# Performance work log

Hardware: AMD Instinct MI355X
Metric: run time of the kernel (lower is better)

Reference implementation:

```python
import jax, jax.numpy as jnp
import numpy as np

WS = 8   # window_size
SS = 4   # shift_size
NH = 4   # num_heads


def _window_partition(x, w):
    B, H, W, C = x.shape
    x = x.reshape(B, H // w, w, W // w, w, C).transpose(0, 1, 3, 2, 4, 5)
    return x.reshape(-1, w, w, C)


def _window_reverse(win, w, H, W):
    B = win.shape[0] // ((H // w) * (W // w))
    x = win.reshape(B, H // w, W // w, w, w, -1).transpose(0, 1, 3, 2, 4, 5)
    return x.reshape(B, H, W, -1)


def _rel_pos_index(w):
    coords = np.stack(np.meshgrid(np.arange(w), np.arange(w), indexing='ij'))  # (2,w,w)
    cf = coords.reshape(2, -1)
    rel = cf[:, :, None] - cf[:, None, :]          # (2,N,N)
    rel = rel.transpose(1, 2, 0)                   # (N,N,2)
    rel[:, :, 0] += w - 1
    rel[:, :, 1] += w - 1
    rel[:, :, 0] *= 2 * w - 1
    return rel.sum(-1)                             # (N,N) int


def _attn_mask(Hp, Wp, w, ss):
    if ss == 0:
        return None
    img = np.zeros((1, Hp, Wp, 1), np.float32)
    slices = (slice(0, -w), slice(-w, -ss), slice(-ss, None))
    cnt = 0
    for h in slices:
        for ww in slices:
            img[:, h, ww, :] = cnt
            cnt += 1
    mw = img.reshape(1, Hp // w, w, Wp // w, w, 1).transpose(0, 1, 3, 2, 4, 5).reshape(-1, w * w)
    m = mw[:, None, :] - mw[:, :, None]
    return np.where(m != 0, -100.0, 0.0).astype(np.float32)  # (nW,N,N)


def _ln(x, g, b, eps=1e-5):
    mu = x.mean(-1, keepdims=True)
    var = ((x - mu) ** 2).mean(-1, keepdims=True)
    return (x - mu) * jax.lax.rsqrt(var + eps) * g + b


def setup_inputs() -> dict:
    key = jax.random.key(0)
    ks = jax.random.split(key, 8)
    B, H, W, C = 4, 256, 256, 128
    hid = 4 * C
    s = 0.02
    return {
        'x': jax.random.normal(ks[0], (B, H * W, C), jnp.float32),
        'norm1_g': jnp.ones((C,), jnp.float32),
        'norm1_b': jnp.zeros((C,), jnp.float32),
        'qkv_w': jax.random.normal(ks[1], (3 * C, C), jnp.float32) * s,
        'qkv_b': jnp.zeros((3 * C,), jnp.float32),
        'rpb_table': jax.random.normal(ks[2], ((2 * WS - 1) ** 2, NH), jnp.float32) * s,
        'proj_w': jax.random.normal(ks[3], (C, C), jnp.float32) * s,
        'proj_b': jnp.zeros((C,), jnp.float32),
        'norm2_g': jnp.ones((C,), jnp.float32),
        'norm2_b': jnp.zeros((C,), jnp.float32),
        'fc1_w': jax.random.normal(ks[4], (hid, C), jnp.float32) * s,
        'fc1_b': jnp.zeros((hid,), jnp.float32),
        'fc2_w': jax.random.normal(ks[5], (C, hid), jnp.float32) * s,
        'fc2_b': jnp.zeros((C,), jnp.float32),
        'H': H,
        'W': W,
    }


def reference(x, norm1_g, norm1_b, qkv_w, qkv_b, rpb_table, proj_w, proj_b,
              norm2_g, norm2_b, fc1_w, fc1_b, fc2_w, fc2_b, H, W):
    B, L, C = x.shape
    hd = C // NH
    scale = hd ** -0.5
    N = WS * WS

    shortcut = x
    h = _ln(x, norm1_g, norm1_b).reshape(B, H, W, C)

    pad_r = (WS - W % WS) % WS
    pad_b = (WS - H % WS) % WS
    if pad_r > 0 or pad_b > 0:
        h = jnp.pad(h, ((0, 0), (0, pad_b), (0, pad_r), (0, 0)))
    Hp, Wp = H + pad_b, W + pad_r

    if SS > 0:
        h = jnp.roll(h, (-SS, -SS), axis=(1, 2))

    win = _window_partition(h, WS).reshape(-1, N, C)   # (B_,N,C)
    B_ = win.shape[0]

    qkv = (win @ qkv_w.T + qkv_b).reshape(B_, N, 3, NH, hd).transpose(2, 0, 3, 1, 4)
    q, k, v = qkv[0] * scale, qkv[1], qkv[2]           # (B_,NH,N,hd)

    attn = jnp.einsum('whnd,whmd->whnm', q, k)         # (B_,NH,N,N)
    rpi = _rel_pos_index(WS).reshape(-1)
    bias = rpb_table[rpi].reshape(N, N, NH).transpose(2, 0, 1)
    attn = attn + bias[None]

    mask = _attn_mask(Hp, Wp, WS, SS)
    if mask is not None:
        nW = mask.shape[0]
        attn = attn.reshape(B_ // nW, nW, NH, N, N) + jnp.asarray(mask)[None, :, None]
        attn = attn.reshape(B_, NH, N, N)

    attn = jax.nn.softmax(attn, axis=-1)
    out = jnp.einsum('whnm,whmd->whnd', attn, v).transpose(0, 2, 1, 3).reshape(B_, N, C)
    out = out @ proj_w.T + proj_b

    out = _window_reverse(out.reshape(-1, WS, WS, C), WS, Hp, Wp)
    if SS > 0:
        out = jnp.roll(out, (SS, SS), axis=(1, 2))
    if pad_r > 0 or pad_b > 0:
        out = out[:, :H, :W, :]
    x = shortcut + out.reshape(B, H * W, C)

    y = _ln(x, norm2_g, norm2_b)
    y = jax.nn.gelu(y @ fc1_w.T + fc1_b, approximate=False) @ fc2_w.T + fc2_b
    return x + y
```

## Files before the change

kernel.cpp:

```cpp
#include <hip/hip_runtime.h>
#include <hip/hip_bf16.h>

typedef unsigned short u16;
typedef unsigned int u32;
typedef __attribute__((ext_vector_type(8))) short bf16x8;
typedef __attribute__((ext_vector_type(4))) float f32x4;

__device__ __forceinline__ u32 fbits(float f) { union { float f; u32 u; } a; a.f = f; return a.u; }
__device__ __forceinline__ u16 f2bf(float f) {
    u32 u = fbits(f);
    return (u16)((u + 0x7FFFu + ((u >> 16) & 1u)) >> 16);
}
__device__ __forceinline__ u16 bfr(float f) { return (u16)((fbits(f) + 0x8000u) >> 16); }
__device__ __forceinline__ u32 pk2(float lo, float hi) {
    return __builtin_amdgcn_perm(fbits(hi) + 0x8000u, fbits(lo) + 0x8000u, 0x07060302u);
}
__device__ __forceinline__ float bf2f(u16 b) {
    union { u32 u; float f; } a; a.u = ((u32)b) << 16; return a.f;
}
__device__ __forceinline__ float gelu_poly(float t) {
    float u = fminf(3.0f, fmaxf(-3.0f, t));
    float u2 = u * u;
    float w = fmaf(u2, 0.00319581f, -0.0550159f);
    w = fmaf(u2, w, 0.401174f);
    float sg = fmaf(u, w, 0.5f);
    return t * sg;
}

#define MFMA(a, b, c) __builtin_amdgcn_mfma_f32_16x16x32_bf16(a, b, c, 0, 0, 0)

__device__ __forceinline__ void gload16(const u16* g, u16* l) {
    __builtin_amdgcn_global_load_lds(
        (const __attribute__((address_space(1))) void*)g,
        (__attribute__((address_space(3))) void*)l, 16, 0, 0);
}

__global__ void swin_prep_kernel(const float* __restrict__ qkv_w, const float* __restrict__ proj_w,
                                 const float* __restrict__ fc1_w, const float* __restrict__ fc2_w,
                                 const float* __restrict__ rpb, u16* __restrict__ wout,
                                 float* __restrict__ bias_lane)
{
    int idx = blockIdx.x * 256 + threadIdx.x;
    if (idx < 49152) wout[idx] = f2bf(qkv_w[idx]);
    else if (idx < 81920) {
        int j = idx - 49152;
        int tile = j >> 9, lane = (j >> 3) & 63, e = j & 7;
        int nt = tile >> 2, ks = tile & 3;
        wout[idx] = f2bf(proj_w[(nt * 16 + (lane & 15)) * 128 + ks * 32 + (lane >> 4) * 8 + e]);
    } else if (idx < 212992) {
        int j = idx - 81920;
        int chunk = j >> 13, rest = j & 8191;
        int tile = rest >> 9, lane = (rest >> 3) & 63, e = rest & 7;
        float v;
        if (tile < 8) {
            int n2 = tile >> 2, ks = tile & 3;
            v = fc1_w[(chunk * 32 + n2 * 16 + (lane & 15)) * 128 + ks * 32 + (lane >> 4) * 8 + e];
        } else {
            int nt = tile - 8;
            v = fc2_w[(nt * 16 + (lane & 15)) * 512 + chunk * 32 + (lane >> 4) * 8 + e];
        }
        wout[idx] = f2bf(v);
    } else {
        int t = idx - 212992;
        int r = t & 3, lane = (t >> 2) & 63, nt = (t >> 8) & 3, mt = (t >> 10) & 3;
        int h = (t >> 12) & 3, v = (t >> 14) & 3;
        int i = mt * 16 + ((lane >> 4) << 2) + r;
        int j = nt * 16 + (lane & 15);
        int ri = i >> 3, ci = i & 7, rj = j >> 3, cj = j & 7;
        int rpi = (ri - rj + 7) * 15 + (ci - cj + 7);
        float bv = rpb[rpi * 4 + h];
        int vh = v >> 1, vw = v & 1;
        int regi = (vh ? (ri < 4 ? 1 : 2) : 0) * 3 + (vw ? (ci < 4 ? 1 : 2) : 0);
        int regj = (vh ? (rj < 4 ? 1 : 2) : 0) * 3 + (vw ? (cj < 4 ? 1 : 2) : 0);
        if (regi != regj) bv -= 100.0f;
        bias_lane[t] = bv * 1.4426950408889634f;
    }
}

__global__ __launch_bounds__(512, 4) void swin_attn_kernel(
    const float* __restrict__ x, const float* __restrict__ g1, const float* __restrict__ b1,
    const float* __restrict__ qkvb, const u16* __restrict__ qkvw,
    const float* __restrict__ bias_lane, u16* __restrict__ attn_out)
{
    __shared__ __align__(16) u16 ldsX[8448];
    __shared__ __align__(16) u16 ldsQK[17408];
    __shared__ float sb[640];

    int tid = threadIdx.x;
    int wid = blockIdx.x;
    int bb_ = wid >> 10, wh = (wid >> 5) & 31, ww = wid & 31;

    for (int i = tid; i < 640; i += 512) {
        float v;
        if (i < 128) v = g1[i];
        else if (i < 256) v = b1[i - 128];
        else v = qkvb[i - 256];
        sb[i] = v;
    }

    int trow = tid >> 3, seg = tid & 7;
    int rn = trow >> 3, cn = trow & 7;
    int srow = (wh * 8 + rn + 4) & 255;
    int scol = (ww * 8 + cn + 4) & 255;
    long grow = (long)bb_ * 65536 + srow * 256 + scol;
    const float4* xrow = (const float4*)(x + grow * 128 + seg * 16);
    float4 xv[4];
    #pragma unroll
    for (int i = 0; i < 4; ++i) xv[i] = xrow[i];
    __syncthreads();

    float s1 = 0.0f, s2 = 0.0f;
    #pragma unroll
    for (int i = 0; i < 4; ++i) {
        float4 v = xv[i];
        s1 += v.x + v.y + v.z + v.w;
        s2 += v.x * v.x + v.y * v.y + v.z * v.z + v.w * v.w;
    }
    #pragma unroll
    for (int off = 1; off < 8; off <<= 1) { s1 += __shfl_xor(s1, off); s2 += __shfl_xor(s2, off); }
    float mu = s1 * 0.0078125f;
    float rstd = rsqrtf(s2 * 0.0078125f - mu * mu + 1e-5f);
    {
        u32 pk[8];
        #pragma unroll
        for (int i = 0; i < 4; ++i) {
            float vv[4] = {xv[i].x, xv[i].y, xv[i].z, xv[i].w};
            float y0, y1, y2, y3;
            {
                int c = seg * 16 + i * 4;
                y0 = (vv[0] - mu) * rstd * sb[c + 0] + sb[128 + c + 0];
                y1 = (vv[1] - mu) * rstd * sb[c + 1] + sb[128 + c + 1];
                y2 = (vv[2] - mu) * rstd * sb[c + 2] + sb[128 + c + 2];
                y3 = (vv[3] - mu) * rstd * sb[c + 3] + sb[128 + c + 3];
            }
            pk[i * 2]     = pk2(y0, y1);
            pk[i * 2 + 1] = pk2(y2, y3);
        }
        *(uint4*)&ldsX[trow * 132 + seg * 16] = *(uint4*)&pk[0];
        *(uint4*)&ldsX[trow * 132 + seg * 16 + 8] = *(uint4*)&pk[4];
    }
    __syncthreads();

    int wave = tid >> 6, lane = tid & 63, l15 = lane & 15, lg = lane >> 4;
    int mrow = lg * 4;
    bf16x8 afr[4][4];
    #pragma unroll
    for (int mt = 0; mt < 4; ++mt)
        #pragma unroll
        for (int ks = 0; ks < 4; ++ks)
            afr[mt][ks] = *(const bf16x8*)&ldsX[(mt * 16 + l15) * 132 + ks * 32 + lg * 8];
    __syncthreads();
    #pragma unroll 1
    for (int nn = 0; nn < 3; ++nn) {
        int nt = wave * 3 + nn;
        int n = nt * 16 + l15;
        const u16* wp = qkvw + n * 128 + lg * 8;
        bf16x8 bfr_[4];
        #pragma unroll
        for (int ks = 0; ks < 4; ++ks) bfr_[ks] = *(const bf16x8*)(wp + ks * 32);
        f32x4 acc[4];
        #pragma unroll
        for (int mt = 0; mt < 4; ++mt) acc[mt] = (f32x4){0.0f, 0.0f, 0.0f, 0.0f};
        #pragma unroll
        for (int ks = 0; ks < 4; ++ks)
            #pragma unroll
            for (int mt = 0; mt < 4; ++mt)
                acc[mt] = MFMA(afr[mt][ks], bfr_[ks], acc[mt]);
        float bias = sb[256 + n];
        if (n < 128) {
            #pragma unroll
            for (int mt = 0; mt < 4; ++mt)
                #pragma unroll
                for (int r = 0; r < 4; ++r)
                    ldsQK[(mt * 16 + mrow + r) * 132 + n] = bfr(acc[mt][r] + bias);
        } else if (n < 256) {
            #pragma unroll
            for (int mt = 0; mt < 4; ++mt)
                #pragma unroll
                for (int r = 0; r < 4; ++r)
                    ldsQK[8448 + (mt * 16 + mrow + r) * 132 + (n - 128)] = bfr(acc[mt][r] + bias);
        } else {
            int row = n - 256;
            int sw = (row & 7) << 4;
            #pragma unroll
            for (int mt = 0; mt < 4; ++mt) {
                uint2 pv;
                pv.x = pk2(acc[mt][0] + bias, acc[mt][1] + bias);
                pv.y = pk2(acc[mt][2] + bias, acc[mt][3] + bias);
                int cb = ((mt * 16 + mrow) * 2) ^ sw;
                *(uint2*)((char*)ldsX + row * 128 + cb) = pv;
            }
        }
    }
    __syncthreads();

    int h = wave >> 1, half = wave & 1;
    int v4 = ((wh == 31) ? 2 : 0) | ((ww == 31) ? 1 : 0);
    const float4* blp = (const float4*)bias_lane;
    bf16x8 bk[4];
    #pragma unroll
    for (int nt = 0; nt < 4; ++nt)
        bk[nt] = *(const bf16x8*)&ldsQK[8448 + (nt * 16 + l15) * 132 + h * 32 + lg * 8];
    f32x4 sS[2][4];
    #pragma unroll
    for (int m2 = 0; m2 < 2; ++m2) {
        int mt = half * 2 + m2;
        bf16x8 aq = *(const bf16x8*)&ldsQK[(mt * 16 + l15) * 132 + h * 32 + lg * 8];
        #pragma unroll
        for (int nt = 0; nt < 4; ++nt) {
            f32x4 z = (f32x4){0.0f, 0.0f, 0.0f, 0.0f};
            z = MFMA(aq, bk[nt], z);
            float4 bl = blp[((v4 * 4 + h) * 16 + mt * 4 + nt) * 64 + lane];
            sS[m2][nt][0] = z[0] * 0.2550349f + bl.x;
            sS[m2][nt][1] = z[1] * 0.2550349f + bl.y;
            sS[m2][nt][2] = z[2] * 0.2550349f + bl.z;
            sS[m2][nt][3] = z[3] * 0.2550349f + bl.w;
        }
    }
    float rinv[2][4];
    #pragma unroll
    for (int m2 = 0; m2 < 2; ++m2) {
        #pragma unroll
        for (int r = 0; r < 4; ++r) {
            float sum = 0.0f;
            #pragma unroll
            for (int nt = 0; nt < 4; ++nt) {
                float p = exp2f(sS[m2][nt][r]);
                sS[m2][nt][r] = p;
                sum += p;
            }
            #pragma unroll
            for (int off = 1; off < 16; off <<= 1) sum += __shfl_xor(sum, off);
            rinv[m2][r] = __builtin_amdgcn_rcpf(sum);
        }
    }
    __syncthreads();
    #pragma unroll
    for (int m2 = 0; m2 < 2; ++m2) {
        int mt = half * 2 + m2;
        #pragma unroll
        for (int nt = 0; nt < 4; ++nt)
            #pragma unroll
            for (int r = 0; r < 4; ++r)
                ldsQK[h * 4352 + (mt * 16 + mrow + r) * 68 + nt * 16 + l15] = bfr(sS[m2][nt][r]);
    }
    __syncthreads();

    f32x4 o[2][2];
    #pragma unroll
    for (int m2 = 0; m2 < 2; ++m2)
        #pragma unroll
        for (int np = 0; np < 2; ++np) o[m2][np] = (f32x4){0.0f, 0.0f, 0.0f, 0.0f};
    #pragma unroll
    for (int kt = 0; kt < 2; ++kt) {
        bf16x8 pa[2];
        #pragma unroll
        for (int m2 = 0; m2 < 2; ++m2) {
            int mt = half * 2 + m2;
            pa[m2] = *(const bf16x8*)&ldsQK[h * 4352 + (mt * 16 + l15) * 68 + kt * 32 + lg * 8];
        }
        #pragma unroll
        for (int np = 0; np < 2; ++np) {
            int vr = h * 32 + np * 16 + l15;
            int cb = (kt * 64 + lg * 16) ^ ((vr & 7) << 4);
            bf16x8 bv = *(const bf16x8*)((const char*)ldsX + vr * 128 + cb);
            #pragma unroll
            for (int m2 = 0; m2 < 2; ++m2)
                o[m2][np] = MFMA(pa[m2], bv, o[m2][np]);
        }
    }
    __syncthreads();
    #pragma unroll
    for (int m2 = 0; m2 < 2; ++m2) {
        int mt = half * 2 + m2;
        #pragma unroll
        for (int np = 0; np < 2; ++np)
            #pragma unroll
            for (int r = 0; r < 4; ++r)
                ldsX[(mt * 16 + mrow + r) * 132 + h * 32 + np * 16 + l15] = bfr(o[m2][np][r] * rinv[m2][r]);
    }
    __syncthreads();
    u16* op = attn_out + grow * 128 + seg * 16;
    *(uint4*)op = *(const uint4*)&ldsX[trow * 132 + seg * 16];
    *(uint4*)(op + 8) = *(const uint4*)&ldsX[trow * 132 + seg * 16 + 8];
}

__global__ __launch_bounds__(256, 3) void swin_mlp_kernel(
    const u16* __restrict__ attn, const float* __restrict__ x,
    const u16* __restrict__ projws, const u16* __restrict__ wms,
    const float* __restrict__ projb, const float* __restrict__ g2, const float* __restrict__ b2,
    const float* __restrict__ f1b, const float* __restrict__ f2b, float* __restrict__ out)
{
    __shared__ __align__(16) u16 wbuf[2][8192];
    __shared__ __align__(16) u16 sbuf[4][1152];

    int tid = threadIdx.x;
    int wave = tid >> 6, lane = tid & 63, l15 = lane & 15, lg = lane >> 4;
    long wbase = (long)blockIdx.x * 128 + wave * 32;

    {
        const u16* src = wms + wave * 2048 + lane * 8;
        u16* dst = &wbuf[0][wave * 2048];
        #pragma unroll
        for (int i = 0; i < 4; ++i)
            gload16(src + i * 512, dst + i * 512);
    }

    const u16* arow = attn + (wbase + l15) * 128 + lg * 8;
    bf16x8 aat[2][4];
    #pragma unroll
    for (int ks = 0; ks < 4; ++ks) {
        aat[0][ks] = *(const bf16x8*)(arow + ks * 32);
        aat[1][ks] = *(const bf16x8*)(arow + 2048 + ks * 32);
    }

    f32x4 pacc[2][8];
    #pragma unroll
    for (int nt = 0; nt < 8; ++nt) {
        const u16* wp = projws + nt * 2048 + lane * 8;
        pacc[0][nt] = (f32x4){0.0f, 0.0f, 0.0f, 0.0f};
        pacc[1][nt] = (f32x4){0.0f, 0.0f, 0.0f, 0.0f};
        #pragma unroll
        for (int ks = 0; ks < 4; ++ks) {
            bf16x8 bw = *(const bf16x8*)(wp + ks * 512);
            pacc[0][nt] = MFMA(aat[0][ks], bw, pacc[0][nt]);
            pacc[1][nt] = MFMA(aat[1][ks], bw, pacc[1][nt]);
        }
    }

    #pragma unroll
    for (int nt = 0; nt < 8; ++nt) {
        float pb = projb[nt * 16 + l15];
        #pragma unroll
        for (int mt = 0; mt < 2; ++mt)
            #pragma unroll
            for (int r = 0; r < 4; ++r)
                pacc[mt][nt][r] += x[(wbase + mt * 16 + lg * 4 + r) * 128 + nt * 16 + l15] + pb;
    }
    float mu[2][4], rstd[2][4];
    #pragma unroll
    for (int mt = 0; mt < 2; ++mt)
        #pragma unroll
        for (int r = 0; r < 4; ++r) {
            float a = 0.0f, bq = 0.0f;
            #pragma unroll
            for (int nt = 0; nt < 8; ++nt) { a += pacc[mt][nt][r]; bq += pacc[mt][nt][r] * pacc[mt][nt][r]; }
            #pragma unroll
            for (int off = 1; off < 16; off <<= 1) { a += __shfl_xor(a, off); bq += __shfl_xor(bq, off); }
            mu[mt][r] = a * 0.0078125f;
            rstd[mt][r] = rsqrtf(bq * 0.0078125f - mu[mt][r] * mu[mt][r] + 1e-5f);
        }
    u16* hb = (u16*)sbuf[wave];
    bf16x8 ay[2][4];
    #pragma unroll
    for (int p = 0; p < 4; ++p) {
        #pragma unroll
        for (int mt = 0; mt < 2; ++mt)
            #pragma unroll
            for (int n2 = 0; n2 < 2; ++n2) {
                int c = p * 32 + n2 * 16 + l15;
                float gg = g2[c], bb = b2[c];
                int nt = p * 2 + n2;
                #pragma unroll
                for (int r = 0; r < 4; ++r)
                    hb[(mt * 16 + lg * 4 + r) * 36 + n2 * 16 + l15] =
                        bfr((pacc[mt][nt][r] - mu[mt][r]) * rstd[mt][r] * gg + bb);
            }
        __builtin_amdgcn_sched_barrier(0);
        ay[0][p] = *(const bf16x8*)&hb[l15 * 36 + lg * 8];
        ay[1][p] = *(const bf16x8*)&hb[(16 + l15) * 36 + lg * 8];
        __builtin_amdgcn_sched_barrier(0);
    }
    #pragma unroll
    for (int nt = 0; nt < 8; ++nt) {
        float fb = f2b[nt * 16 + l15];
        #pragma unroll
        for (int mt = 0; mt < 2; ++mt)
            #pragma unroll
            for (int r = 0; r < 4; ++r)
                pacc[mt][nt][r] += fb;
    }
    __syncthreads();

    #pragma unroll 1
    for (int cc = 0; cc < 16; ++cc) {
        int cur = cc & 1;
        if (cc < 15) {
            const u16* src = wms + (cc + 1) * 8192 + wave * 2048 + lane * 8;
            u16* dst = &wbuf[cur ^ 1][wave * 2048];
            #pragma unroll
            for (int i = 0; i < 4; ++i)
                gload16(src + i * 512, dst + i * 512);
        }
        f32x4 h[2][2];
        h[0][0] = h[0][1] = h[1][0] = h[1][1] = (f32x4){0.0f, 0.0f, 0.0f, 0.0f};
        #pragma unroll
        for (int n2 = 0; n2 < 2; ++n2)
            #pragma unroll
            for (int ks = 0; ks < 4; ++ks) {
                bf16x8 bw = *(const bf16x8*)&wbuf[cur][(n2 * 4 + ks) * 512 + lane * 8];
                h[0][n2] = MFMA(ay[0][ks], bw, h[0][n2]);
                h[1][n2] = MFMA(ay[1][ks], bw, h[1][n2]);
            }
        #pragma unroll
        for (int n2 = 0; n2 < 2; ++n2) {
            float fb = f1b[cc * 32 + n2 * 16 + l15];
            #pragma unroll
            for (int mt = 0; mt < 2; ++mt)
                #pragma unroll
                for (int r = 0; r < 4; ++r) {
                    float ge = gelu_poly(h[mt][n2][r] + fb);
                    hb[(mt * 16 + lg * 4 + r) * 36 + n2 * 16 + l15] = bfr(ge);
                }
        }
        __builtin_amdgcn_sched_barrier(0);
        bf16x8 ah0 = *(const bf16x8*)&hb[l15 * 36 + lg * 8];
        bf16x8 ah1 = *(const bf16x8*)&hb[(16 + l15) * 36 + lg * 8];
        __builtin_amdgcn_sched_barrier(0);
        #pragma unroll
        for (int nt = 0; nt < 8; ++nt) {
            bf16x8 bw = *(const bf16x8*)&wbuf[cur][(8 + nt) * 512 + lane * 8];
            pacc[0][nt] = MFMA(ah0, bw, pacc[0][nt]);
            pacc[1][nt] = MFMA(ah1, bw, pacc[1][nt]);
        }
        __syncthreads();
    }
    #pragma unroll
    for (int nt = 0; nt < 8; ++nt)
        #pragma unroll
        for (int mt = 0; mt < 2; ++mt)
            #pragma unroll
            for (int r = 0; r < 4; ++r)
                out[(wbase + mt * 16 + lg * 4 + r) * 128 + nt * 16 + l15] = pacc[mt][nt][r];
}

extern "C" void kernel_launch(void* const* d_in, const int* in_sizes, int n_in,
                              void* d_out, int out_size, void* d_ws, size_t ws_size,
                              hipStream_t stream)
{
    const float* x     = (const float*)d_in[0];
    const float* n1g   = (const float*)d_in[1];
    const float* n1b   = (const float*)d_in[2];
    const float* qkvw  = (const float*)d_in[3];
    const float* qkvb  = (const float*)d_in[4];
    const float* rpb   = (const float*)d_in[5];
    const float* projw = (const float*)d_in[6];
    const float* projb = (const float*)d_in[7];
    const float* n2g   = (const float*)d_in[8];
    const float* n2b   = (const float*)d_in[9];
    const float* f1w   = (const float*)d_in[10];
    const float* f1b   = (const float*)d_in[11];
    const float* f2w   = (const float*)d_in[12];
    const float* f2b   = (const float*)d_in[13];

    char* ws = (char*)d_ws;
    u16* attn_buf = (u16*)ws;
    u16* wb = (u16*)(ws + 67108864);
    float* bias_lane = (float*)(ws + 67108864 + 425984);
    u16* qkvwb  = wb;
    u16* projws = wb + 49152;
    u16* wms    = wb + 81920;

    swin_prep_kernel<<<1088, 256, 0, stream>>>(qkvw, projw, f1w, f2w, rpb, wb, bias_lane);
    swin_attn_kernel<<<4096, 512, 0, stream>>>(x, n1g, n1b, qkvb, qkvwb, bias_lane, attn_buf);
    swin_mlp_kernel<<<2048, 256, 0, stream>>>(attn_buf, x, projws, wms,
                                              projb, n2g, n2b, f1b, f2b, (float*)d_out);
}
```

Baseline: 247.5 us.

## Compute fc1 transposed so GELU output feeds fc2 MFMA from registers

Swaps the fc1 MFMA operands so each lane's accumulator holds the hidden-unit values it needs as the A operand of the fc2 MFMA. The fc2 weights are re-permuted in the prep kernel to match the new k ordering. This removes the per-chunk LDS write/read round trip for the GELU activations and halves the per-wave staging buffer. It relies on the permuted weight layout matching the MFMA register mapping exactly.

```diff
diff --git a/kernel.cpp b/kernel.cpp
--- a/kernel.cpp
+++ b/kernel.cpp
@@ -51,13 +51,15 @@
         int j = idx - 81920;
         int chunk = j >> 13, rest = j & 8191;
         int tile = rest >> 9, lane = (rest >> 3) & 63, e = rest & 7;
+        int lg = lane >> 4;
         float v;
         if (tile < 8) {
-            int n2 = tile >> 2, ks = tile & 3;
-            v = fc1_w[(chunk * 32 + n2 * 16 + (lane & 15)) * 128 + ks * 32 + (lane >> 4) * 8 + e];
+            int mh = tile >> 2, ks = tile & 3;
+            v = fc1_w[(chunk * 32 + mh * 16 + (lane & 15)) * 128 + ks * 32 + lg * 8 + e];
         } else {
             int nt = tile - 8;
-            v = fc2_w[(nt * 16 + (lane & 15)) * 512 + chunk * 32 + (lane >> 4) * 8 + e];
+            int hid = (e < 4) ? (lg * 4 + e) : (16 + lg * 4 + (e - 4));
+            v = fc2_w[(nt * 16 + (lane & 15)) * 512 + chunk * 32 + hid];
         }
         wout[idx] = f2bf(v);
     } else {
@@ -292,7 +294,7 @@
     const float* __restrict__ f1b, const float* __restrict__ f2b, float* __restrict__ out)
 {
     __shared__ __align__(16) u16 wbuf[2][8192];
-    __shared__ __align__(16) u16 sbuf[4][1152];
+    __shared__ __align__(16) u16 sbuf[4][576];
 
     int tid = threadIdx.x;
     int wave = tid >> 6, lane = tid & 63, l15 = lane & 15, lg = lane >> 4;
@@ -355,7 +357,7 @@
     #pragma unroll
     for (int p = 0; p < 4; ++p) {
         #pragma unroll
-        for (int mt = 0; mt < 2; ++mt)
+        for (int mt = 0; mt < 2; ++mt) {
             #pragma unroll
             for (int n2 = 0; n2 < 2; ++n2) {
                 int c = p * 32 + n2 * 16 + l15;
@@ -363,13 +365,13 @@
                 int nt = p * 2 + n2;
                 #pragma unroll
                 for (int r = 0; r < 4; ++r)
-                    hb[(mt * 16 + lg * 4 + r) * 36 + n2 * 16 + l15] =
+                    hb[(lg * 4 + r) * 36 + n2 * 16 + l15] =
                         bfr((pacc[mt][nt][r] - mu[mt][r]) * rstd[mt][r] * gg + bb);
             }
-        __builtin_amdgcn_sched_barrier(0);
-        ay[0][p] = *(const bf16x8*)&hb[l15 * 36 + lg * 8];
-        ay[1][p] = *(const bf16x8*)&hb[(16 + l15) * 36 + lg * 8];
-        __builtin_amdgcn_sched_barrier(0);
+            __builtin_amdgcn_sched_barrier(0);
+            ay[mt][p] = *(const bf16x8*)&hb[l15 * 36 + lg * 8];
+            __builtin_amdgcn_sched_barrier(0);
+        }
     }
     #pragma unroll
     for (int nt = 0; nt < 8; ++nt) {
@@ -395,33 +397,38 @@
         f32x4 h[2][2];
         h[0][0] = h[0][1] = h[1][0] = h[1][1] = (f32x4){0.0f, 0.0f, 0.0f, 0.0f};
         #pragma unroll
-        for (int n2 = 0; n2 < 2; ++n2)
+        for (int mh = 0; mh < 2; ++mh)
             #pragma unroll
             for (int ks = 0; ks < 4; ++ks) {
-                bf16x8 bw = *(const bf16x8*)&wbuf[cur][(n2 * 4 + ks) * 512 + lane * 8];
-                h[0][n2] = MFMA(ay[0][ks], bw, h[0][n2]);
-                h[1][n2] = MFMA(ay[1][ks], bw, h[1][n2]);
-            }
-        #pragma unroll
-        for (int n2 = 0; n2 < 2; ++n2) {
-            float fb = f1b[cc * 32 + n2 * 16 + l15];
-            #pragma unroll
-            for (int mt = 0; mt < 2; ++mt)
-                #pragma unroll
-                for (int r = 0; r < 4; ++r) {
-                    float ge = gelu_poly(h[mt][n2][r] + fb);
-                    hb[(mt * 16 + lg * 4 + r) * 36 + n2 * 16 + l15] = bfr(ge);
-                }
-        }
-        __builtin_amdgcn_sched_barrier(0);
-        bf16x8 ah0 = *(const bf16x8*)&hb[l15 * 36 + lg * 8];
-        bf16x8 ah1 = *(const bf16x8*)&hb[(16 + l15) * 36 + lg * 8];
-        __builtin_amdgcn_sched_barrier(0);
+                bf16x8 w1 = *(const bf16x8*)&wbuf[cur][(mh * 4 + ks) * 512 + lane * 8];
+                h[0][mh] = MFMA(w1, ay[0][ks], h[0][mh]);
+                h[1][mh] = MFMA(w1, ay[1][ks], h[1][mh]);
+            }
+        float4 fb0 = *(const float4*)(f1b + cc * 32 + lg * 4);
+        float4 fb1 = *(const float4*)(f1b + cc * 32 + 16 + lg * 4);
+        float b0[4] = {fb0.x, fb0.y, fb0.z, fb0.w};
+        float b1[4] = {fb1.x, fb1.y, fb1.z, fb1.w};
+        bf16x8 ah[2];
+        #pragma unroll
+        for (int mt = 0; mt < 2; ++mt) {
+            float g0[4], g1[4];
+            #pragma unroll
+            for (int r = 0; r < 4; ++r) {
+                g0[r] = gelu_poly(h[mt][0][r] + b0[r]);
+                g1[r] = gelu_poly(h[mt][1][r] + b1[r]);
+            }
+            union { u32 w[4]; bf16x8 v; } u_;
+            u_.w[0] = pk2(g0[0], g0[1]);
+            u_.w[1] = pk2(g0[2], g0[3]);
+            u_.w[2] = pk2(g1[0], g1[1]);
+            u_.w[3] = pk2(g1[2], g1[3]);
+            ah[mt] = u_.v;
+        }
         #pragma unroll
         for (int nt = 0; nt < 8; ++nt) {
             bf16x8 bw = *(const bf16x8*)&wbuf[cur][(8 + nt) * 512 + lane * 8];
-            pacc[0][nt] = MFMA(ah0, bw, pacc[0][nt]);
-            pacc[1][nt] = MFMA(ah1, bw, pacc[1][nt]);
+            pacc[0][nt] = MFMA(ah[0], bw, pacc[0][nt]);
+            pacc[1][nt] = MFMA(ah[1], bw, pacc[1][nt]);
         }
         __syncthreads();
     }
```

Measured after the change: 235.1 us. 1.05x faster.
